# Performance work log

Measured on AMD Instinct MI355X. Metric: run time of the kernel, lower is better.

The kernel has to match this reference:

```python
import jax, jax.numpy as jnp
import numpy as np
from jax import lax

K = 3          # kernel_size
STRIDE = 1
DN = ('NHWC', 'HWIO', 'NHWC')


def setup_inputs() -> dict:
    key = jax.random.key(0)
    k1, k2, k3 = jax.random.split(key, 3)
    inputs = jax.random.normal(k1, (8, 256, 256, 3), dtype=jnp.float32)
    # truncated-normal-ish init, stddev 0.1
    w_mu = 0.1 * jax.random.truncated_normal(k2, -2.0, 2.0, (K, K, 3, 128), dtype=jnp.float32)
    w_sigma = jax.random.uniform(k3, (128,), minval=-12.0, maxval=-4.6, dtype=jnp.float32)
    return {"inputs": inputs, "w_mu": w_mu, "w_sigma": w_sigma}


def reference(inputs, w_mu, w_sigma):
    # mean path: standard conv2d
    mu_out = lax.conv_general_dilated(inputs, w_mu, (STRIDE, STRIDE), 'VALID',
                                      dimension_numbers=DN)
    # variance path: original code does (x_patches**2) @ broadcast(softplus(w_sigma)).
    # Since vect_sigma is constant along the patch dimension, this equals
    # sum-over-patch(x^2) * softplus(w_sigma)[c]. Compute sum-pool via a ones conv,
    # avoiding materializing the huge im2col patch tensor.
    sp_sigma = jax.nn.softplus(w_sigma)                      # [Cout]
    cin = inputs.shape[-1]
    ones_k = jnp.ones((K, K, cin, 1), dtype=inputs.dtype)
    sumsq = lax.conv_general_dilated(inputs * inputs, ones_k, (STRIDE, STRIDE),
                                     'VALID', dimension_numbers=DN)  # [N,H',W',1]
    sigma_out = sumsq * sp_sigma                              # broadcast -> [N,H',W',Cout]
    return mu_out, sigma_out
```

## Files before the change

### kernel.cpp

```cpp
#include <hip/hip_runtime.h>
#include <hip/hip_fp16.h>
#include <math.h>

#define H_IN   256
#define W_IN   256
#define CIN    3
#define COUT   128
#define NB     8
#define KS     3
#define H_OUT  254
#define W_OUT  254
#define ROW_F  (W_IN * CIN)

typedef float f32x4 __attribute__((ext_vector_type(4)));

#define FMA_MIX_LO(acc, wp, xv) \
    asm("v_fma_mix_f32 %0, %1, %2, %0 op_sel:[0,0,0] op_sel_hi:[1,0,0]" \
        : "+v"(acc) : "v"(wp), "v"(xv))
#define FMA_MIX_HI(acc, wp, xv) \
    asm("v_fma_mix_f32 %0, %1, %2, %0 op_sel:[1,0,0] op_sel_hi:[1,0,0]" \
        : "+v"(acc) : "v"(wp), "v"(xv))

__global__ __launch_bounds__(256, 4)
void conv_meanvar_kernel(const float* __restrict__ in,
                         const float* __restrict__ w_mu,
                         const float* __restrict__ w_sigma,
                         float* __restrict__ out)
{
    __shared__ float lds[3 * ROW_F + 32];

    const int h   = blockIdx.x;
    const int n   = blockIdx.y;
    const int tid = threadIdx.x;
    const int px  = tid >> 5;
    const int c4  = (tid & 31) * 4;

    const float* src = in + (size_t)(n * H_IN + h) * ROW_F;
    if (tid < 144) {
        const f32x4* s4 = reinterpret_cast<const f32x4*>(src) + tid * 4;
        f32x4* d4 = reinterpret_cast<f32x4*>(lds) + tid * 4;
        d4[0] = s4[0]; d4[1] = s4[1]; d4[2] = s4[2]; d4[3] = s4[3];
    }

    unsigned int wpk[27][2];
    #pragma unroll
    for (int kk = 0; kk < 27; ++kk) {
        f32x4 w = *reinterpret_cast<const f32x4*>(w_mu + kk * COUT + c4);
        wpk[kk][0] = (unsigned int)__half_as_ushort(__float2half(w.x))
                   | ((unsigned int)__half_as_ushort(__float2half(w.y)) << 16);
        wpk[kk][1] = (unsigned int)__half_as_ushort(__float2half(w.z))
                   | ((unsigned int)__half_as_ushort(__float2half(w.w)) << 16);
    }

    f32x4 ws = *reinterpret_cast<const f32x4*>(w_sigma + c4);
    float sp[4];
    sp[0] = log1pf(expf(ws.x));
    sp[1] = log1pf(expf(ws.y));
    sp[2] = log1pf(expf(ws.z));
    sp[3] = log1pf(expf(ws.w));

    __syncthreads();

    const size_t pix_base = (size_t)(n * H_OUT + h) * W_OUT;
    float* const out_sig  = out + (size_t)NB * H_OUT * W_OUT * COUT;

    #pragma unroll 1
    for (int it = 0; it < 8; ++it) {
        const int p0 = it * 32 + px * 4;

        float mu[4][4];
        float ss[4];
        #pragma unroll
        for (int j = 0; j < 4; ++j) {
            ss[j] = 0.f;
            mu[j][0] = mu[j][1] = mu[j][2] = mu[j][3] = 0.f;
        }

        #pragma unroll
        for (int kh = 0; kh < KS; ++kh) {
            const f32x4* rq = reinterpret_cast<const f32x4*>(
                                  &lds[kh * ROW_F + p0 * 3]);
            float r[20];
            *reinterpret_cast<f32x4*>(&r[0])  = rq[0];
            *reinterpret_cast<f32x4*>(&r[4])  = rq[1];
            *reinterpret_cast<f32x4*>(&r[8])  = rq[2];
            *reinterpret_cast<f32x4*>(&r[12]) = rq[3];
            *reinterpret_cast<f32x4*>(&r[16]) = rq[4];

            #pragma unroll
            for (int j = 0; j < 4; ++j) {
                #pragma unroll
                for (int q = 0; q < 9; ++q) {
                    const float x = r[j * 3 + q];
                    const int kk = kh * 9 + q;
                    FMA_MIX_LO(mu[j][0], wpk[kk][0], x);
                    FMA_MIX_HI(mu[j][1], wpk[kk][0], x);
                    FMA_MIX_LO(mu[j][2], wpk[kk][1], x);
                    FMA_MIX_HI(mu[j][3], wpk[kk][1], x);
                    ss[j] = fmaf(x, x, ss[j]);
                }
            }
        }

        #pragma unroll
        for (int j = 0; j < 4; ++j) {
            const int p = p0 + j;
            if (p < W_OUT) {
                const size_t o = (pix_base + p) * COUT + c4;
                f32x4 m = {mu[j][0], mu[j][1], mu[j][2], mu[j][3]};
                __builtin_nontemporal_store(m, reinterpret_cast<f32x4*>(out + o));
            }
        }
        #pragma unroll
        for (int j = 0; j < 4; ++j) {
            const int p = p0 + j;
            if (p < W_OUT) {
                const size_t o = (pix_base + p) * COUT + c4;
                f32x4 sg = {ss[j] * sp[0], ss[j] * sp[1],
                            ss[j] * sp[2], ss[j] * sp[3]};
                __builtin_nontemporal_store(sg, reinterpret_cast<f32x4*>(out_sig + o));
            }
        }
    }
}

extern "C" void kernel_launch(void* const* d_in, const int* in_sizes, int n_in,
                              void* d_out, int out_size, void* d_ws, size_t ws_size,
                              hipStream_t stream)
{
    const float* in      = (const float*)d_in[0];
    const float* w_mu    = (const float*)d_in[1];
    const float* w_sigma = (const float*)d_in[2];
    float* out           = (float*)d_out;

    dim3 grid(H_OUT, NB);
    dim3 block(256);
    conv_meanvar_kernel<<<grid, block, 0, stream>>>(in, w_mu, w_sigma, out);
}
```

Measured before the change: 116.9 us.

## Process four output rows per block with 512 threads and shared halo rows

Each block now loads six input rows into LDS and computes four output rows, so the two halo rows are reused instead of reloaded by neighbouring blocks. Per-block setup (fp16 weight packing, softplus) is amortized over more work, and the block grows to 512 threads with a 64-pixel stride per iteration. The mean and sigma stores are interleaved per pixel. In exchange, the grid shrinks to 64x8 blocks, which may underfill the GPU's CUs, and the larger LDS footprint and launch bounds may limit occupancy.

```diff
diff --git a/kernel.cpp b/kernel.cpp
--- a/kernel.cpp
+++ b/kernel.cpp
@@ -11,6 +11,8 @@
 #define H_OUT  254
 #define W_OUT  254
 #define ROW_F  (W_IN * CIN)
+#define ROWS_PB 4
+#define NGH    ((H_OUT + ROWS_PB - 1) / ROWS_PB)
 
 typedef float f32x4 __attribute__((ext_vector_type(4)));
 
@@ -21,25 +23,29 @@
     asm("v_fma_mix_f32 %0, %1, %2, %0 op_sel:[1,0,0] op_sel_hi:[1,0,0]" \
         : "+v"(acc) : "v"(wp), "v"(xv))
 
-__global__ __launch_bounds__(256, 4)
+__global__ __launch_bounds__(512, 4)
 void conv_meanvar_kernel(const float* __restrict__ in,
                          const float* __restrict__ w_mu,
                          const float* __restrict__ w_sigma,
                          float* __restrict__ out)
 {
-    __shared__ float lds[3 * ROW_F + 32];
+    __shared__ float lds[(ROWS_PB + 2) * ROW_F + 32];
 
-    const int h   = blockIdx.x;
+    const int gh  = blockIdx.x;
     const int n   = blockIdx.y;
     const int tid = threadIdx.x;
     const int px  = tid >> 5;
     const int c4  = (tid & 31) * 4;
 
-    const float* src = in + (size_t)(n * H_IN + h) * ROW_F;
-    if (tid < 144) {
-        const f32x4* s4 = reinterpret_cast<const f32x4*>(src) + tid * 4;
-        f32x4* d4 = reinterpret_cast<f32x4*>(lds) + tid * 4;
-        d4[0] = s4[0]; d4[1] = s4[1]; d4[2] = s4[2]; d4[3] = s4[3];
+    const int h0 = gh * ROWS_PB;
+    const int nr = min(ROWS_PB, H_OUT - h0);
+
+    {
+        const f32x4* s4 = reinterpret_cast<const f32x4*>(
+                              in + (size_t)(n * H_IN + h0) * ROW_F);
+        f32x4* d4 = reinterpret_cast<f32x4*>(lds);
+        const int nvec = (nr + 2) * (ROW_F / 4);
+        for (int i = tid; i < nvec; i += 512) d4[i] = s4[i];
     }
 
     unsigned int wpk[27][2];
@@ -61,64 +67,62 @@
 
     __syncthreads();
 
-    const size_t pix_base = (size_t)(n * H_OUT + h) * W_OUT;
-    float* const out_sig  = out + (size_t)NB * H_OUT * W_OUT * COUT;
+    float* const out_sig = out + (size_t)NB * H_OUT * W_OUT * COUT;
 
     #pragma unroll 1
-    for (int it = 0; it < 8; ++it) {
-        const int p0 = it * 32 + px * 4;
+    for (int r = 0; r < nr; ++r) {
+        const size_t pix_base = (size_t)(n * H_OUT + h0 + r) * W_OUT;
+        const float* rowbase = lds + r * ROW_F;
 
-        float mu[4][4];
-        float ss[4];
-        #pragma unroll
-        for (int j = 0; j < 4; ++j) {
-            ss[j] = 0.f;
-            mu[j][0] = mu[j][1] = mu[j][2] = mu[j][3] = 0.f;
-        }
+        #pragma unroll 1
+        for (int it = 0; it < 4; ++it) {
+            const int p0 = it * 64 + px * 4;
 
-        #pragma unroll
-        for (int kh = 0; kh < KS; ++kh) {
-            const f32x4* rq = reinterpret_cast<const f32x4*>(
-                                  &lds[kh * ROW_F + p0 * 3]);
-            float r[20];
-            *reinterpret_cast<f32x4*>(&r[0])  = rq[0];
-            *reinterpret_cast<f32x4*>(&r[4])  = rq[1];
-            *reinterpret_cast<f32x4*>(&r[8])  = rq[2];
-            *reinterpret_cast<f32x4*>(&r[12]) = rq[3];
-            *reinterpret_cast<f32x4*>(&r[16]) = rq[4];
+            float mu[4][4];
+            float ss[4];
+            #pragma unroll
+            for (int j = 0; j < 4; ++j) {
+                ss[j] = 0.f;
+                mu[j][0] = mu[j][1] = mu[j][2] = mu[j][3] = 0.f;
+            }
+
+            #pragma unroll
+            for (int kh = 0; kh < KS; ++kh) {
+                const f32x4* rq = reinterpret_cast<const f32x4*>(
+                                      rowbase + kh * ROW_F + p0 * 3);
+                float rr[20];
+                *reinterpret_cast<f32x4*>(&rr[0])  = rq[0];
+                *reinterpret_cast<f32x4*>(&rr[4])  = rq[1];
+                *reinterpret_cast<f32x4*>(&rr[8])  = rq[2];
+                *reinterpret_cast<f32x4*>(&rr[12]) = rq[3];
+                *reinterpret_cast<f32x4*>(&rr[16]) = rq[4];
+
+                #pragma unroll
+                for (int j = 0; j < 4; ++j) {
+                    #pragma unroll
+                    for (int q = 0; q < 9; ++q) {
+                        const float x = rr[j * 3 + q];
+                        const int kk = kh * 9 + q;
+                        FMA_MIX_LO(mu[j][0], wpk[kk][0], x);
+                        FMA_MIX_HI(mu[j][1], wpk[kk][0], x);
+                        FMA_MIX_LO(mu[j][2], wpk[kk][1], x);
+                        FMA_MIX_HI(mu[j][3], wpk[kk][1], x);
+                        ss[j] = fmaf(x, x, ss[j]);
+                    }
+                }
+            }
 
             #pragma unroll
             for (int j = 0; j < 4; ++j) {
-                #pragma unroll
-                for (int q = 0; q < 9; ++q) {
-                    const float x = r[j * 3 + q];
-                    const int kk = kh * 9 + q;
-                    FMA_MIX_LO(mu[j][0], wpk[kk][0], x);
-                    FMA_MIX_HI(mu[j][1], wpk[kk][0], x);
-                    FMA_MIX_LO(mu[j][2], wpk[kk][1], x);
-                    FMA_MIX_HI(mu[j][3], wpk[kk][1], x);
-                    ss[j] = fmaf(x, x, ss[j]);
+                const int p = p0 + j;
+                if (p < W_OUT) {
+                    const size_t o = (pix_base + p) * COUT + c4;
+                    f32x4 m = {mu[j][0], mu[j][1], mu[j][2], mu[j][3]};
+                    __builtin_nontemporal_store(m, reinterpret_cast<f32x4*>(out + o));
+                    f32x4 sg = {ss[j] * sp[0], ss[j] * sp[1],
+                                ss[j] * sp[2], ss[j] * sp[3]};
+                    __builtin_nontemporal_store(sg, reinterpret_cast<f32x4*>(out_sig + o));
                 }
-            }
-        }
-
-        #pragma unroll
-        for (int j = 0; j < 4; ++j) {
-            const int p = p0 + j;
-            if (p < W_OUT) {
-                const size_t o = (pix_base + p) * COUT + c4;
-                f32x4 m = {mu[j][0], mu[j][1], mu[j][2], mu[j][3]};
-                __builtin_nontemporal_store(m, reinterpret_cast<f32x4*>(out + o));
-            }
-        }
-        #pragma unroll
-        for (int j = 0; j < 4; ++j) {
-            const int p = p0 + j;
-            if (p < W_OUT) {
-                const size_t o = (pix_base + p) * COUT + c4;
-                f32x4 sg = {ss[j] * sp[0], ss[j] * sp[1],
-                            ss[j] * sp[2], ss[j] * sp[3]};
-                __builtin_nontemporal_store(sg, reinterpret_cast<f32x4*>(out_sig + o));
             }
         }
     }
@@ -133,7 +137,7 @@
     const float* w_sigma = (const float*)d_in[2];
     float* out           = (float*)d_out;
 
-    dim3 grid(H_OUT, NB);
-    dim3 block(256);
+    dim3 grid(NGH, NB);
+    dim3 block(512);
     conv_meanvar_kernel<<<grid, block, 0, stream>>>(in, w_mu, w_sigma, out);
 }
```

After: 122.9 us. +5.1%, slower.

## Split fused conv into separate mean and sigma kernels

Applied to the files above, without the earlier changes.

The fused kernel is split into two launches. One computes the mean convolution. The other computes the per-pixel sum of squares once per row into shared memory, then broadcasts it across output channels. The sum-of-squares work is no longer repeated in every thread for every channel group, and nontemporal stores are replaced with regular stores. In exchange the input rows are loaded twice, there is an extra kernel launch, and the two output streams are written in separate passes rather than interleaved.

```diff
diff --git a/kernel.cpp b/kernel.cpp
--- a/kernel.cpp
+++ b/kernel.cpp
@@ -22,10 +22,9 @@
         : "+v"(acc) : "v"(wp), "v"(xv))
 
 __global__ __launch_bounds__(256, 4)
-void conv_meanvar_kernel(const float* __restrict__ in,
-                         const float* __restrict__ w_mu,
-                         const float* __restrict__ w_sigma,
-                         float* __restrict__ out)
+void mu_kernel(const float* __restrict__ in,
+               const float* __restrict__ w_mu,
+               float* __restrict__ out)
 {
     __shared__ float lds[3 * ROW_F + 32];
 
@@ -52,29 +51,18 @@
                    | ((unsigned int)__half_as_ushort(__float2half(w.w)) << 16);
     }
 
-    f32x4 ws = *reinterpret_cast<const f32x4*>(w_sigma + c4);
-    float sp[4];
-    sp[0] = log1pf(expf(ws.x));
-    sp[1] = log1pf(expf(ws.y));
-    sp[2] = log1pf(expf(ws.z));
-    sp[3] = log1pf(expf(ws.w));
-
     __syncthreads();
 
     const size_t pix_base = (size_t)(n * H_OUT + h) * W_OUT;
-    float* const out_sig  = out + (size_t)NB * H_OUT * W_OUT * COUT;
 
     #pragma unroll 1
     for (int it = 0; it < 8; ++it) {
         const int p0 = it * 32 + px * 4;
 
         float mu[4][4];
-        float ss[4];
         #pragma unroll
-        for (int j = 0; j < 4; ++j) {
-            ss[j] = 0.f;
+        for (int j = 0; j < 4; ++j)
             mu[j][0] = mu[j][1] = mu[j][2] = mu[j][3] = 0.f;
-        }
 
         #pragma unroll
         for (int kh = 0; kh < KS; ++kh) {
@@ -97,7 +85,6 @@
                     FMA_MIX_HI(mu[j][1], wpk[kk][0], x);
                     FMA_MIX_LO(mu[j][2], wpk[kk][1], x);
                     FMA_MIX_HI(mu[j][3], wpk[kk][1], x);
-                    ss[j] = fmaf(x, x, ss[j]);
                 }
             }
         }
@@ -108,17 +95,70 @@
             if (p < W_OUT) {
                 const size_t o = (pix_base + p) * COUT + c4;
                 f32x4 m = {mu[j][0], mu[j][1], mu[j][2], mu[j][3]};
-                __builtin_nontemporal_store(m, reinterpret_cast<f32x4*>(out + o));
+                *reinterpret_cast<f32x4*>(out + o) = m;
             }
         }
+    }
+}
+
+__global__ __launch_bounds__(256, 8)
+void sigma_kernel(const float* __restrict__ in,
+                  const float* __restrict__ w_sigma,
+                  float* __restrict__ out_sig)
+{
+    __shared__ float lds[3 * ROW_F + 32];
+    __shared__ float ssrow[W_OUT + 2];
+
+    const int h   = blockIdx.x;
+    const int n   = blockIdx.y;
+    const int tid = threadIdx.x;
+    const int px  = tid >> 5;
+    const int c4  = (tid & 31) * 4;
+
+    const float* src = in + (size_t)(n * H_IN + h) * ROW_F;
+    if (tid < 144) {
+        const f32x4* s4 = reinterpret_cast<const f32x4*>(src) + tid * 4;
+        f32x4* d4 = reinterpret_cast<f32x4*>(lds) + tid * 4;
+        d4[0] = s4[0]; d4[1] = s4[1]; d4[2] = s4[2]; d4[3] = s4[3];
+    }
+
+    f32x4 ws = *reinterpret_cast<const f32x4*>(w_sigma + c4);
+    float sp[4];
+    sp[0] = log1pf(expf(ws.x));
+    sp[1] = log1pf(expf(ws.y));
+    sp[2] = log1pf(expf(ws.z));
+    sp[3] = log1pf(expf(ws.w));
+
+    __syncthreads();
+
+    if (tid < W_OUT) {
+        const int base = tid * 3;
+        float s = 0.f;
+        #pragma unroll
+        for (int kh = 0; kh < KS; ++kh) {
+            #pragma unroll
+            for (int q = 0; q < 9; ++q) {
+                const float x = lds[kh * ROW_F + base + q];
+                s = fmaf(x, x, s);
+            }
+        }
+        ssrow[tid] = s;
+    }
+    __syncthreads();
+
+    const size_t pix_base = (size_t)(n * H_OUT + h) * W_OUT;
+
+    #pragma unroll 1
+    for (int it = 0; it < 8; ++it) {
+        const int p0 = it * 32 + px * 4;
         #pragma unroll
         for (int j = 0; j < 4; ++j) {
             const int p = p0 + j;
             if (p < W_OUT) {
+                const float ss = ssrow[p];
                 const size_t o = (pix_base + p) * COUT + c4;
-                f32x4 sg = {ss[j] * sp[0], ss[j] * sp[1],
-                            ss[j] * sp[2], ss[j] * sp[3]};
-                __builtin_nontemporal_store(sg, reinterpret_cast<f32x4*>(out_sig + o));
+                f32x4 sg = {ss * sp[0], ss * sp[1], ss * sp[2], ss * sp[3]};
+                *reinterpret_cast<f32x4*>(out_sig + o) = sg;
             }
         }
     }
@@ -132,8 +172,10 @@
     const float* w_mu    = (const float*)d_in[1];
     const float* w_sigma = (const float*)d_in[2];
     float* out           = (float*)d_out;
+    float* out_sig       = out + (size_t)NB * H_OUT * W_OUT * COUT;
 
     dim3 grid(H_OUT, NB);
     dim3 block(256);
-    conv_meanvar_kernel<<<grid, block, 0, stream>>>(in, w_mu, w_sigma, out);
+    mu_kernel<<<grid, block, 0, stream>>>(in, w_mu, out);
+    sigma_kernel<<<grid, block, 0, stream>>>(in, w_sigma, out_sig);
 }
```

Result: slower. 131.1 us (+12.1%).
